# Optimization experiments

Hardware: AMD Instinct MI355X
Metric: run time of the kernel (lower is better)

## Reference

```python
import jax, jax.numpy as jnp
import numpy as np

B, N, V, D, C, H = 2, 4096, 4, 256, 3, 512


def setup_inputs() -> dict:
    key = jax.random.key(0)
    ks = jax.random.split(key, 8)
    desc = jax.random.normal(ks[0], (B, N, V, D), dtype=jnp.float32)
    sf = jax.random.normal(ks[1], (B, N, V, C), dtype=jnp.float32)
    T = jax.random.normal(ks[2], (V, 4, 4), dtype=jnp.float32)
    W1 = jax.random.normal(ks[3], (D, H), dtype=jnp.float32) * 0.05
    b1 = jnp.zeros((H,), dtype=jnp.float32)
    Wt = jax.random.normal(ks[4], (32, H), dtype=jnp.float32) * 0.05
    W2 = jax.random.normal(ks[5], (H, C), dtype=jnp.float32) * 0.05
    b2 = jnp.zeros((C,), dtype=jnp.float32)
    return {"desc": desc, "sf": sf, "T": T, "W1": W1, "b1": b1, "Wt": Wt, "W2": W2, "b2": b2}


def reference(desc, sf, T, W1, b1, Wt, W2, b2):
    # desc: [B,N,V,D], sf: [B,N,V,C], T: [V,4,4]
    Bn, Nn, Vn, Dn = desc.shape
    eps = 1e-12
    mutual = jnp.arange(Nn)[None, :]  # [1,N]

    def recon(d_i, Ti, Tj):
        # kpnet.reconstruction proxy: 2-layer MLP conditioned on flattened poses
        tcode = jnp.concatenate([Ti.ravel(), Tj.ravel()]) @ Wt  # [H]
        h = jax.nn.relu(d_i @ W1 + tcode + b1)                  # [B,N,H]
        return h @ W2 + b2                                      # [B,N,C]

    loss_total = jnp.float32(0.0)
    count = jnp.float32(0.0)
    for i in range(Vn):
        for j in range(Vn):
            if i == j:
                continue
            di = desc[:, :, i, :]  # [B,N,D]
            dj = desc[:, :, j, :]
            din = di / jnp.maximum(jnp.linalg.norm(di, axis=-1, keepdims=True), eps)
            djn = dj / jnp.maximum(jnp.linalg.norm(dj, axis=-1, keepdims=True), eps)
            sim_n = jnp.einsum('bnd,bmd->bnm', din, djn)  # [B,N,N]
            idx_ij = jnp.argmax(sim_n, axis=2)            # [B,N]
            idx_ji = jnp.argmax(sim_n, axis=1)            # [B,N]
            back = jnp.take_along_axis(idx_ji, idx_ij, axis=1)
            has_mutual = jnp.sum(back == mutual, axis=1) > 0  # [B]

            sf_recon = recon(di, T[i], T[j])              # [B,N,C]
            sim = jnp.einsum('bnd,bmd->bnm', di, dj)      # unnormalized, matches no_grad branch
            prob = jax.nn.softmax(sim, axis=2)
            sf_j_soft = jax.lax.stop_gradient(jnp.einsum('bnm,bmc->bnc', prob, sf[:, :, j, :]))
            loss_b = jnp.mean((sf_recon - sf_j_soft) ** 2, axis=(1, 2))  # [B]

            loss_total = loss_total + jnp.sum(jnp.where(has_mutual, loss_b, 0.0))
            count = count + jnp.sum(has_mutual.astype(jnp.float32))

    fallback = 0.0 * (W1.sum() + W2.sum() + Wt.sum() + b1.sum() + b2.sum())
    return jnp.where(count > 0, loss_total / jnp.maximum(count, 1.0), fallback)
```

## Files before the change

### kernel.cpp

```cpp
#include <hip/hip_runtime.h>
#include <cstdint>
#include <cstddef>

#define N_ 4096
#define B_ 2
#define V_ 4
#define D_ 256
#define C_ 3
#define H_ 512

#define PLANE 1048576
#define WPLANE 131072
#define NEG_INF (-__builtin_inff())
#define TSTRIDE 130

typedef __attribute__((ext_vector_type(8))) _Float16 f16x8;
typedef __attribute__((ext_vector_type(4))) float f32x4;

__device__ __forceinline__ void gload16(const void* g, void* l) {
    __builtin_amdgcn_global_load_lds(
        (const __attribute__((address_space(1))) void*)g,
        (__attribute__((address_space(3))) void*)l,
        16, 0, 0);
}

__device__ __forceinline__ void split2(float x, unsigned short& h, unsigned short& l) {
    _Float16 hh = (_Float16)x;
    float r = x - (float)hh;
    _Float16 ll = (_Float16)r;
    h = __builtin_bit_cast(unsigned short, hh);
    l = __builtin_bit_cast(unsigned short, ll);
}

__device__ __forceinline__ size_t sp_idx(int n, int d) {
    int R = n >> 4, rr = n & 15;
    int Kc = d >> 5, slot = (d >> 3) & 3, e = d & 7;
    return ((((size_t)R * 8 + Kc) * 4 + slot) * 16 + rr) * 8 + e;
}

__global__ __launch_bounds__(64) void zero_accum_kernel(float* loss_sum, int* hm) {
    int t = threadIdx.x;
    if (t < 24) loss_sum[t] = 0.0f;
    if (t < 12) hm[t] = 0;
}

__global__ __launch_bounds__(256) void split_kernel(const float* __restrict__ desc,
                                                    unsigned short* __restrict__ SP) {
    int t = blockIdx.x * 256 + threadIdx.x;
    int d4 = t & 63;
    int v  = (t >> 6) & 3;
    int n  = (t >> 8) & 4095;
    int b  = t >> 20;
    const float4 x = *(const float4*)(desc + (((size_t)(b * N_ + n) * V_ + v) << 8) + d4 * 4);
    ushort4 hv, lv;
    split2(x.x, hv.x, lv.x);
    split2(x.y, hv.y, lv.y);
    split2(x.z, hv.z, lv.z);
    split2(x.w, hv.w, lv.w);
    size_t base = (size_t)((b * V_ + v) * 2) * PLANE + sp_idx(n, d4 * 4);
    *(ushort4*)(SP + base)         = hv;
    *(ushort4*)(SP + base + PLANE) = lv;
}

__global__ __launch_bounds__(256) void w1split_kernel(const float* __restrict__ W1,
                                                      unsigned short* __restrict__ W1T) {
    int t = blockIdx.x * 256 + threadIdx.x;
    int h = t & 511;
    int k = t >> 9;
    float x = W1[(size_t)k * H_ + h];
    unsigned short hv, lv;
    split2(x, hv, lv);
    size_t o = sp_idx(h, k);
    W1T[o] = hv; W1T[o + WPLANE] = lv;
}

__global__ __launch_bounds__(256) void norms_kernel(const float* __restrict__ desc,
                                                    float* __restrict__ invn) {
    int gw   = (blockIdx.x * 256 + threadIdx.x) >> 6;
    int lane = threadIdx.x & 63;
    int bv = gw >> 12;
    int n  = gw & (N_ - 1);
    int b  = bv >> 2, v = bv & 3;
    const float* p = desc + ((size_t)(b * N_ + n) * V_ + v) * D_;
    float4 x = *(const float4*)(p + lane * 4);
    float s = x.x * x.x + x.y * x.y + x.z * x.z + x.w * x.w;
    #pragma unroll
    for (int off = 32; off >= 1; off >>= 1) s += __shfl_xor(s, off, 64);
    if (lane == 0) invn[gw] = 1.0f / fmaxf(sqrtf(s), 1e-12f);
}

__global__ __launch_bounds__(256) void fgram_kernel(
    const unsigned short* __restrict__ SP,
    const float* __restrict__ sf,
    const float* __restrict__ invn,
    float* __restrict__ PT) {
    __shared__ __align__(16) unsigned char smraw[49152];
    __shared__ float wmax[4];
    unsigned short* stage = (unsigned short*)smraw;
    float* tile  = (float*)smraw;
    float* CSb   = (float*)(smraw + 33280);
    float4* sfj4 = (float4*)(smraw + 37888);
    float4* sfi4 = (float4*)(smraw + 41984);

    const int tid = threadIdx.x;
    const int wid = tid >> 6, lane = tid & 63;
    const int wr = wid >> 1, wc = wid & 1;
    const int g = lane >> 4, ccol = lane & 15;

    const int pi[6] = {0, 0, 0, 1, 1, 2}, pj[6] = {1, 2, 3, 2, 3, 3};
    const int u = blockIdx.y, b = u & 1;
    const int i = pi[u >> 1], j = pj[u >> 1];
    float* RP = PT + (size_t)u * 64 * N_ * 8;
    float* CP = RP + (size_t)32 * N_ * 8;

    const int bid = blockIdx.x;
    const int swz = (bid & 7) * 64 + (bid >> 3);
    const int strip = swz >> 4, chunk = swz & 15;
    const int n0 = strip * 128, m0 = chunk * 256;

    const unsigned short* Ahi = SP + (size_t)((b * V_ + i) * 2 + 0) * PLANE;
    const unsigned short* Alo = Ahi + PLANE;
    const unsigned short* Bhi = SP + (size_t)((b * V_ + j) * 2 + 0) * PLANE;
    const unsigned short* Blo = Bhi + PLANE;
    const int gA = b * V_ + i, gB = b * V_ + j;

    const int q = wid * 2;

    for (int t = 0; t < 2; ++t) {
        const int brow0 = m0 + t * 128;
        const int RA0 = n0 >> 4, RB0 = brow0 >> 4;

        f32x4 acc[4][4];
        #pragma unroll
        for (int m = 0; m < 4; ++m)
            #pragma unroll
            for (int n = 0; n < 4; ++n) acc[m][n] = (f32x4){0.f, 0.f, 0.f, 0.f};

        for (int k0 = 0; k0 < D_; k0 += 32) {
            const int Kc = k0 >> 5;
            __syncthreads();
            const unsigned short* planes[4] = {Ahi, Alo, Bhi, Blo};
            #pragma unroll
            for (int pl = 0; pl < 4; ++pl) {
                const int R0 = (pl < 2) ? RA0 : RB0;
                #pragma unroll
                for (int c = 0; c < 2; ++c) {
                    const unsigned short* gp =
                        planes[pl] + (((size_t)(R0 + q + c) * 8 + Kc) * 512) + lane * 8;
                    gload16(gp, stage + pl * 4096 + (q + c) * 512);
                }
            }
            __syncthreads();

            const int funit = (g * 16 + ccol) * 8;
            f16x8 ah[4], al4[4], bh[4];
            #pragma unroll
            for (int m = 0; m < 4; ++m) {
                ah[m]  = *(const f16x8*)(stage + 0 * 4096 + (wr * 4 + m) * 512 + funit);
                al4[m] = *(const f16x8*)(stage + 1 * 4096 + (wr * 4 + m) * 512 + funit);
                bh[m]  = *(const f16x8*)(stage + 2 * 4096 + (wc * 4 + m) * 512 + funit);
            }
            #pragma unroll
            for (int m = 0; m < 4; ++m)
                #pragma unroll
                for (int n = 0; n < 4; ++n)
                    acc[m][n] = __builtin_amdgcn_mfma_f32_16x16x32_f16(
                        ah[m], bh[n], acc[m][n], 0, 0, 0);
            #pragma unroll
            for (int m = 0; m < 4; ++m)
                #pragma unroll
                for (int n = 0; n < 4; ++n)
                    acc[m][n] = __builtin_amdgcn_mfma_f32_16x16x32_f16(
                        al4[m], bh[n], acc[m][n], 0, 0, 0);
            f16x8 bl4[4];
            #pragma unroll
            for (int n = 0; n < 4; ++n)
                bl4[n] = *(const f16x8*)(stage + 3 * 4096 + (wc * 4 + n) * 512 + funit);
            #pragma unroll
            for (int m = 0; m < 4; ++m)
                #pragma unroll
                for (int n = 0; n < 4; ++n)
                    acc[m][n] = __builtin_amdgcn_mfma_f32_16x16x32_f16(
                        ah[m], bl4[n], acc[m][n], 0, 0, 0);
        }

        float tmax = NEG_INF;
        #pragma unroll
        for (int m = 0; m < 4; ++m)
            #pragma unroll
            for (int n = 0; n < 4; ++n)
                #pragma unroll
                for (int r = 0; r < 4; ++r)
                    tmax = fmaxf(tmax, acc[m][n][r]);
        #pragma unroll
        for (int off = 1; off <= 32; off <<= 1)
            tmax = fmaxf(tmax, __shfl_xor(tmax, off, 64));
        if (lane == 0) wmax[wid] = tmax;
        __syncthreads();
        const float mxt = fmaxf(fmaxf(wmax[0], wmax[1]), fmaxf(wmax[2], wmax[3]));

        {
            if (tid < 128) {
                int m = m0 + t * 128 + tid;
                const float* p = sf + (((size_t)(b * N_ + m)) * V_ + j) * C_;
                sfj4[tid] = make_float4(p[0], p[1], p[2], invn[(size_t)gB * N_ + m]);
            } else {
                int n = n0 + (tid & 127);
                const float* p = sf + (((size_t)(b * N_ + n)) * V_ + i) * C_;
                sfi4[tid & 127] = make_float4(p[0], p[1], p[2], invn[(size_t)gA * N_ + n]);
            }
        }

        for (int half = 0; half < 2; ++half) {
            if (wr == half) {
                #pragma unroll
                for (int m = 0; m < 4; ++m)
                    #pragma unroll
                    for (int nf = 0; nf < 4; ++nf) {
                        int c = wc * 64 + nf * 16 + ccol;
                        int rb = m * 16 + g * 4;
                        #pragma unroll
                        for (int r = 0; r < 4; ++r)
                            tile[(rb + r) * TSTRIDE + c] = acc[m][nf][r];
                    }
            }
            __syncthreads();

            {
                const int row = tid >> 2, qq = tid & 3;
                const float* rp = tile + row * TSTRIDE;
                float sum = 0.f, w0 = 0.f, w1 = 0.f, w2 = 0.f;
                float bv = NEG_INF, bif = (float)N_;
                for (int ii = 0; ii < 32; ++ii) {
                    int c = (ii << 2) + qq;
                    float s = rp[c];
                    float4 sp = sfj4[c];
                    float e = __expf(s - mxt);
                    sum += e;
                    w0 = fmaf(e, sp.x, w0); w1 = fmaf(e, sp.y, w1); w2 = fmaf(e, sp.z, w2);
                    float vv = s * sp.w;
                    float gi = (float)(m0 + t * 128 + c);
                    if (vv > bv || (vv == bv && gi < bif)) { bv = vv; bif = gi; }
                }
                #pragma unroll
                for (int off = 1; off <= 2; off <<= 1) {
                    sum += __shfl_xor(sum, off, 64);
                    w0  += __shfl_xor(w0, off, 64);
                    w1  += __shfl_xor(w1, off, 64);
                    w2  += __shfl_xor(w2, off, 64);
                    float ob = __shfl_xor(bv, off, 64);
                    float oi = __shfl_xor(bif, off, 64);
                    if (ob > bv || (ob == bv && oi < bif)) { bv = ob; bif = oi; }
                }
                if (qq == 0) {
                    float* o = RP + ((size_t)(chunk * 2 + t) * N_ + n0 + half * 64 + row) * 8;
                    *(float4*)o       = make_float4(mxt, sum, w0, w1);
                    *(float4*)(o + 4) = make_float4(w2, bv, bif, 0.f);
                }
            }

            {
                const int c = tid >> 1, h = tid & 1;
                const float* cp = tile + (h * 32) * TSTRIDE + c;
                const int rb0 = half * 64 + h * 32;
                float sum = 0.f, w0 = 0.f, w1 = 0.f, w2 = 0.f;
                float bv = NEG_INF, bif = (float)N_;
                for (int ii = 0; ii < 32; ++ii) {
                    float s = cp[ii * TSTRIDE];
                    float4 sp = sfi4[rb0 + ii];
                    float e = __expf(s - mxt);
                    sum += e;
                    w0 = fmaf(e, sp.x, w0); w1 = fmaf(e, sp.y, w1); w2 = fmaf(e, sp.z, w2);
                    float vv = s * sp.w;
                    float gi = (float)(n0 + rb0 + ii);
                    if (vv > bv || (vv == bv && gi < bif)) { bv = vv; bif = gi; }
                }
                {
                    sum += __shfl_xor(sum, 1, 64);
                    w0  += __shfl_xor(w0, 1, 64);
                    w1  += __shfl_xor(w1, 1, 64);
                    w2  += __shfl_xor(w2, 1, 64);
                    float ob = __shfl_xor(bv, 1, 64);
                    float oi = __shfl_xor(bif, 1, 64);
                    if (ob > bv || (ob == bv && oi < bif)) { bv = ob; bif = oi; }
                }
                if (h == 0) {
                    float* cs = CSb + c * 9;
                    if (half == 0) {
                        cs[0] = sum; cs[1] = w0; cs[2] = w1; cs[3] = w2;
                        cs[4] = bv;  cs[5] = bif;
                    } else {
                        cs[0] += sum; cs[1] += w0; cs[2] += w1; cs[3] += w2;
                        if (bv > cs[4] || (bv == cs[4] && bif < cs[5])) { cs[4] = bv; cs[5] = bif; }
                    }
                }
            }
            __syncthreads();
        }

        if (tid < 128) {
            const float* cs = CSb + tid * 9;
            float* o = CP + ((size_t)strip * N_ + m0 + t * 128 + tid) * 8;
            *(float4*)o       = make_float4(mxt, cs[0], cs[1], cs[2]);
            *(float4*)(o + 4) = make_float4(cs[3], cs[4], cs[5], 0.f);
        }
    }
}

__global__ __launch_bounds__(256) void comb_kernel(const float* __restrict__ PT,
                                                   float* __restrict__ soft,
                                                   int* __restrict__ idxbuf) {
    const int pi[6] = {0, 0, 0, 1, 1, 2}, pj[6] = {1, 2, 3, 2, 3, 3};
    int u = blockIdx.y, p = u >> 1, b = u & 1;
    int i = pi[p], j = pj[p];
    int x = blockIdx.x;
    int idx = (x & 15) * 256 + threadIdx.x;
    const size_t unit = (size_t)u * 64 * N_ * 8;
    const float* base;
    int dd, which;
    if (x < 16) { base = PT + unit + (size_t)idx * 8;                       dd = (i * 3 + (j - 1)) * 2 + b; which = 0; }
    else        { base = PT + unit + (size_t)32 * N_ * 8 + (size_t)idx * 8; dd = (j * 3 + i) * 2 + b;       which = 1; }

    float4 a = *(const float4*)base;
    float4 b4 = *(const float4*)(base + 4);
    float M = a.x, S = a.y, w0 = a.z, w1 = a.w, w2 = b4.x, av = b4.y, ai = b4.z;
    for (int k = 1; k < 32; ++k) {
        const float* qp = base + (size_t)k * N_ * 8;
        float4 c = *(const float4*)qp;
        float4 d = *(const float4*)(qp + 4);
        if (c.x > M) {
            float e = __expf(M - c.x);
            M = c.x;
            S  = fmaf(S,  e, c.y);
            w0 = fmaf(w0, e, c.z);
            w1 = fmaf(w1, e, c.w);
            w2 = fmaf(w2, e, d.x);
        } else {
            float e = __expf(c.x - M);
            S  = fmaf(c.y, e, S);
            w0 = fmaf(c.z, e, w0);
            w1 = fmaf(c.w, e, w1);
            w2 = fmaf(d.x, e, w2);
        }
        if (d.y > av || (d.y == av && d.z < ai)) { av = d.y; ai = d.z; }
    }
    float inv = 1.0f / S;
    float* so = soft + ((size_t)dd * N_ + idx) * 3;
    so[0] = w0 * inv; so[1] = w1 * inv; so[2] = w2 * inv;
    idxbuf[((size_t)u * 2 + which) * N_ + idx] = (int)ai;
}

__global__ __launch_bounds__(256) void mutualB_kernel(const int* __restrict__ idxbuf,
                                                      int* __restrict__ hm) {
    int u = blockIdx.y;
    int n = blockIdx.x * 256 + threadIdx.x;
    int a = idxbuf[((size_t)u * 2 + 0) * N_ + n];
    int ok = (idxbuf[((size_t)u * 2 + 1) * N_ + a] == n) ? 1 : 0;
    unsigned long long m = __ballot(ok);
    if ((threadIdx.x & 63) == 0 && m != 0ull) atomicOr(&hm[u], 1);
}

__global__ __launch_bounds__(256) void zmm3_kernel(const unsigned short* __restrict__ SP,
                                                   const unsigned short* __restrict__ W1T,
                                                   const float* __restrict__ b1,
                                                   float* __restrict__ Z) {
    __shared__ __align__(16) unsigned short stage[4 * 4096];
    const int tid = threadIdx.x;
    const int wid = tid >> 6, lane = tid & 63;
    const int wr = wid >> 1, wc = wid & 1;
    const int g = lane >> 4, ccol = lane & 15;
    const int bv = blockIdx.z;
    const int arow0 = blockIdx.x * 128, bcol0 = blockIdx.y * 128;
    const int RA0 = arow0 >> 4, RB0 = bcol0 >> 4;

    const unsigned short* Ahi = SP + (size_t)(bv * 2) * PLANE;
    const unsigned short* Alo = Ahi + PLANE;
    const unsigned short* Bhi = W1T;
    const unsigned short* Blo = W1T + WPLANE;
    float* Cout = Z + (size_t)bv * N_ * H_;

    f32x4 acc[4][4];
    #pragma unroll
    for (int m = 0; m < 4; ++m)
        #pragma unroll
        for (int n = 0; n < 4; ++n) acc[m][n] = (f32x4){0.f, 0.f, 0.f, 0.f};

    const int q = wid * 2;

    for (int k0 = 0; k0 < D_; k0 += 32) {
        const int Kc = k0 >> 5;
        __syncthreads();
        const unsigned short* planes[4] = {Ahi, Alo, Bhi, Blo};
        #pragma unroll
        for (int pl = 0; pl < 4; ++pl) {
            const int R0 = (pl < 2) ? RA0 : RB0;
            #pragma unroll
            for (int c = 0; c < 2; ++c) {
                const unsigned short* gp =
                    planes[pl] + (((size_t)(R0 + q + c) * 8 + Kc) * 512) + lane * 8;
                gload16(gp, stage + pl * 4096 + (q + c) * 512);
            }
        }
        __syncthreads();

        const int funit = (g * 16 + ccol) * 8;
        f16x8 ah[4], al4[4], bh[4];
        #pragma unroll
        for (int m = 0; m < 4; ++m) {
            ah[m]  = *(const f16x8*)(stage + 0 * 4096 + (wr * 4 + m) * 512 + funit);
            al4[m] = *(const f16x8*)(stage + 1 * 4096 + (wr * 4 + m) * 512 + funit);
            bh[m]  = *(const f16x8*)(stage + 2 * 4096 + (wc * 4 + m) * 512 + funit);
        }
        #pragma unroll
        for (int m = 0; m < 4; ++m)
            #pragma unroll
            for (int n = 0; n < 4; ++n)
                acc[m][n] = __builtin_amdgcn_mfma_f32_16x16x32_f16(ah[m], bh[n], acc[m][n], 0, 0, 0);
        #pragma unroll
        for (int m = 0; m < 4; ++m)
            #pragma unroll
            for (int n = 0; n < 4; ++n)
                acc[m][n] = __builtin_amdgcn_mfma_f32_16x16x32_f16(al4[m], bh[n], acc[m][n], 0, 0, 0);
        f16x8 bl4[4];
        #pragma unroll
        for (int n = 0; n < 4; ++n)
            bl4[n] = *(const f16x8*)(stage + 3 * 4096 + (wc * 4 + n) * 512 + funit);
        #pragma unroll
        for (int m = 0; m < 4; ++m)
            #pragma unroll
            for (int n = 0; n < 4; ++n)
                acc[m][n] = __builtin_amdgcn_mfma_f32_16x16x32_f16(ah[m], bl4[n], acc[m][n], 0, 0, 0);
    }

    const int crow = (lane >> 4) * 4;
    #pragma unroll
    for (int m = 0; m < 4; ++m) {
        const int gr = arow0 + wr * 64 + m * 16 + crow;
        #pragma unroll
        for (int n = 0; n < 4; ++n) {
            const int gc = bcol0 + wc * 64 + n * 16 + ccol;
            f32x4 v = acc[m][n];
            float bvx = b1[gc];
            #pragma unroll
            for (int r = 0; r < 4; ++r)
                Cout[(size_t)(gr + r) * H_ + gc] = v[r] + bvx;
        }
    }
}

__global__ __launch_bounds__(512) void tcode_kernel(const float* __restrict__ T,
                                                    const float* __restrict__ Wt,
                                                    float* __restrict__ tcode) {
    int dp = blockIdx.x;
    int i = dp / 3, rem = dp % 3;
    int j = rem + (rem >= i ? 1 : 0);
    int h = threadIdx.x;
    float acc = 0.0f;
    #pragma unroll
    for (int k = 0; k < 16; k++) acc = fmaf(T[i * 16 + k], Wt[k * H_ + h], acc);
    #pragma unroll
    for (int k = 0; k < 16; k++) acc = fmaf(T[j * 16 + k], Wt[(16 + k) * H_ + h], acc);
    tcode[dp * H_ + h] = acc;
}

__global__ __launch_bounds__(256) void loss_kernel(const float* __restrict__ Z,
                                                   const float* __restrict__ tcode,
                                                   const float* __restrict__ soft,
                                                   const float* __restrict__ W2,
                                                   const float* __restrict__ b2,
                                                   float* __restrict__ loss_sum) {
    int dd = blockIdx.y;
    int dp = dd >> 1, b = dd & 1;
    int i = dp / 3;
    const float* tc = tcode + (size_t)dp * H_;
    const float* zbase = Z + (size_t)((b * V_ + i) * N_) * H_;
    const float* softb = soft + (size_t)dd * N_ * C_;
    int tid = threadIdx.x;
    int wid = tid >> 6, lane = tid & 63;
    __shared__ float wsum[4];
    float sse_acc = 0.0f;
    float4 t1 = *(const float4*)(tc + lane * 4);
    float4 t2 = *(const float4*)(tc + 256 + lane * 4);
    for (int rr = wid; rr < 64; rr += 4) {
        int n = blockIdx.x * 64 + rr;
        const float* zp = zbase + (size_t)n * H_;
        float4 z1 = *(const float4*)(zp + lane * 4);
        float4 z2 = *(const float4*)(zp + 256 + lane * 4);
        float pre[8] = {z1.x + t1.x, z1.y + t1.y, z1.z + t1.z, z1.w + t1.w,
                        z2.x + t2.x, z2.y + t2.y, z2.z + t2.z, z2.w + t2.w};
        float c0 = 0.f, c1 = 0.f, c2 = 0.f;
        int h1 = lane * 4, h2 = 256 + lane * 4;
        #pragma unroll
        for (int q = 0; q < 8; q++) {
            float rv = fmaxf(pre[q], 0.0f);
            int h = (q < 4) ? (h1 + q) : (h2 + q - 4);
            c0 = fmaf(rv, W2[h * 3 + 0], c0);
            c1 = fmaf(rv, W2[h * 3 + 1], c1);
            c2 = fmaf(rv, W2[h * 3 + 2], c2);
        }
        #pragma unroll
        for (int off = 32; off >= 1; off >>= 1) {
            c0 += __shfl_xor(c0, off, 64);
            c1 += __shfl_xor(c1, off, 64);
            c2 += __shfl_xor(c2, off, 64);
        }
        if (lane == 0) {
            float e0 = c0 + b2[0] - softb[(size_t)n * C_ + 0];
            float e1 = c1 + b2[1] - softb[(size_t)n * C_ + 1];
            float e2 = c2 + b2[2] - softb[(size_t)n * C_ + 2];
            sse_acc += e0 * e0 + e1 * e1 + e2 * e2;
        }
    }
    if (lane == 0) wsum[wid] = sse_acc;
    __syncthreads();
    if (tid == 0) {
        atomicAdd(&loss_sum[dd], wsum[0] + wsum[1] + wsum[2] + wsum[3]);
    }
}

__global__ __launch_bounds__(64) void final_kernel(const float* __restrict__ loss_sum,
                                                   const int* __restrict__ hm,
                                                   float* __restrict__ out) {
    if (threadIdx.x != 0 || blockIdx.x != 0) return;
    float lt = 0.0f, cnt = 0.0f;
    for (int dp = 0; dp < 12; dp++) {
        int i = dp / 3, rem = dp % 3;
        int j = rem + (rem >= i ? 1 : 0);
        int a = i < j ? i : j, c = i < j ? j : i;
        int p = a * 3 - (a * (a - 1)) / 2 + (c - a - 1);
        for (int b = 0; b < 2; b++) {
            if (hm[p * 2 + b]) {
                lt += loss_sum[dp * 2 + b] * (1.0f / ((float)N_ * (float)C_));
                cnt += 1.0f;
            }
        }
    }
    out[0] = (cnt > 0.0f) ? (lt / cnt) : 0.0f;
}

extern "C" void kernel_launch(void* const* d_in, const int* in_sizes, int n_in,
                              void* d_out, int out_size, void* d_ws, size_t ws_size,
                              hipStream_t stream) {
    const float* desc = (const float*)d_in[0];
    const float* sf   = (const float*)d_in[1];
    const float* T    = (const float*)d_in[2];
    const float* W1   = (const float*)d_in[3];
    const float* b1   = (const float*)d_in[4];
    const float* Wt   = (const float*)d_in[5];
    const float* W2   = (const float*)d_in[6];
    const float* b2   = (const float*)d_in[7];
    float* out = (float*)d_out;

    const size_t NM = (size_t)N_ * N_;
    unsigned short* SP  = (unsigned short*)d_ws;
    unsigned short* W1T = SP + (size_t)16 * PLANE;
    float* w     = (float*)(W1T + (size_t)2 * WPLANE);
    float* Z     = w;
    float* PT    = w + NM;
    float* invn  = PT + (size_t)12 * 64 * N_ * 8;
    float* tcode = invn + (size_t)B_ * V_ * N_;
    float* soft  = tcode + 12 * H_;
    int*   idxbuf = (int*)(soft + (size_t)12 * B_ * N_ * C_);
    float* loss_sum = (float*)(idxbuf + (size_t)12 * 2 * N_);
    int*   hm    = (int*)(loss_sum + 24);

    zero_accum_kernel<<<1, 64, 0, stream>>>(loss_sum, hm);
    split_kernel<<<8192, 256, 0, stream>>>(desc, SP);
    w1split_kernel<<<512, 256, 0, stream>>>(W1, W1T);
    norms_kernel<<<(B_ * V_ * N_) / 4, 256, 0, stream>>>(desc, invn);
    tcode_kernel<<<12, 512, 0, stream>>>(T, Wt, tcode);

    fgram_kernel<<<dim3(512, 12), 256, 0, stream>>>(SP, sf, invn, PT);

    zmm3_kernel<<<dim3(32, 4, 8), 256, 0, stream>>>(SP, W1T, b1, Z);
    comb_kernel<<<dim3(32, 12), 256, 0, stream>>>(PT, soft, idxbuf);
    mutualB_kernel<<<dim3(16, 12), 256, 0, stream>>>(idxbuf, hm);
    loss_kernel<<<dim3(64, 24), 256, 0, stream>>>(Z, tcode, soft, W2, b2, loss_sum);
    final_kernel<<<1, 64, 0, stream>>>(loss_sum, hm, out);
}
```

Before: 1.172 ms.

## Double K-step staging in fgram and reuse exponentials for column softmax

Widens the K chunk staged per sync from 32 to 64, halving the number of barrier-separated load/compute rounds. Shared memory grows to about 64KB of dynamic LDS, which may reduce occupancy. The row pass now writes exp values back into the tile so the column pass reuses them instead of recomputing expf. The column argmax is computed from the register accumulators with warp shuffles instead of from the shared tile, at the cost of an extra barrier.

```diff
diff --git a/kernel.cpp b/kernel.cpp
--- a/kernel.cpp
+++ b/kernel.cpp
@@ -94,13 +94,13 @@
     const float* __restrict__ sf,
     const float* __restrict__ invn,
     float* __restrict__ PT) {
-    __shared__ __align__(16) unsigned char smraw[49152];
-    __shared__ float wmax[4];
+    extern __shared__ __align__(16) unsigned char smraw[];
     unsigned short* stage = (unsigned short*)smraw;
     float* tile  = (float*)smraw;
     float* CSb   = (float*)(smraw + 33280);
     float4* sfj4 = (float4*)(smraw + 37888);
     float4* sfi4 = (float4*)(smraw + 41984);
+    float* wmax  = (float*)(smraw + 65536);
 
     const int tid = threadIdx.x;
     const int wid = tid >> 6, lane = tid & 63;
@@ -136,52 +136,57 @@
             #pragma unroll
             for (int n = 0; n < 4; ++n) acc[m][n] = (f32x4){0.f, 0.f, 0.f, 0.f};
 
-        for (int k0 = 0; k0 < D_; k0 += 32) {
-            const int Kc = k0 >> 5;
+        for (int k0 = 0; k0 < D_; k0 += 64) {
+            const int Kc0 = k0 >> 5;
             __syncthreads();
             const unsigned short* planes[4] = {Ahi, Alo, Bhi, Blo};
             #pragma unroll
             for (int pl = 0; pl < 4; ++pl) {
                 const int R0 = (pl < 2) ? RA0 : RB0;
                 #pragma unroll
-                for (int c = 0; c < 2; ++c) {
+                for (int c = 0; c < 4; ++c) {
+                    const int rowg = q + (c >> 1);
+                    const int kc = c & 1;
                     const unsigned short* gp =
-                        planes[pl] + (((size_t)(R0 + q + c) * 8 + Kc) * 512) + lane * 8;
-                    gload16(gp, stage + pl * 4096 + (q + c) * 512);
+                        planes[pl] + (((size_t)(R0 + rowg) * 8 + Kc0 + kc) * 512) + lane * 8;
+                    gload16(gp, stage + pl * 8192 + (rowg * 2 + kc) * 512);
                 }
             }
             __syncthreads();
 
             const int funit = (g * 16 + ccol) * 8;
-            f16x8 ah[4], al4[4], bh[4];
-            #pragma unroll
-            for (int m = 0; m < 4; ++m) {
-                ah[m]  = *(const f16x8*)(stage + 0 * 4096 + (wr * 4 + m) * 512 + funit);
-                al4[m] = *(const f16x8*)(stage + 1 * 4096 + (wr * 4 + m) * 512 + funit);
-                bh[m]  = *(const f16x8*)(stage + 2 * 4096 + (wc * 4 + m) * 512 + funit);
-            }
-            #pragma unroll
-            for (int m = 0; m < 4; ++m)
+            #pragma unroll
+            for (int kk2 = 0; kk2 < 2; ++kk2) {
+                f16x8 ah[4], al4[4], bh4[4];
+                #pragma unroll
+                for (int m = 0; m < 4; ++m) {
+                    ah[m]  = *(const f16x8*)(stage + 0 * 8192 + ((wr * 4 + m) * 2 + kk2) * 512 + funit);
+                    al4[m] = *(const f16x8*)(stage + 1 * 8192 + ((wr * 4 + m) * 2 + kk2) * 512 + funit);
+                    bh4[m] = *(const f16x8*)(stage + 2 * 8192 + ((wc * 4 + m) * 2 + kk2) * 512 + funit);
+                }
+                #pragma unroll
+                for (int m = 0; m < 4; ++m)
+                    #pragma unroll
+                    for (int n = 0; n < 4; ++n)
+                        acc[m][n] = __builtin_amdgcn_mfma_f32_16x16x32_f16(
+                            ah[m], bh4[n], acc[m][n], 0, 0, 0);
+                #pragma unroll
+                for (int m = 0; m < 4; ++m)
+                    #pragma unroll
+                    for (int n = 0; n < 4; ++n)
+                        acc[m][n] = __builtin_amdgcn_mfma_f32_16x16x32_f16(
+                            al4[m], bh4[n], acc[m][n], 0, 0, 0);
+                f16x8 bl4[4];
                 #pragma unroll
                 for (int n = 0; n < 4; ++n)
-                    acc[m][n] = __builtin_amdgcn_mfma_f32_16x16x32_f16(
-                        ah[m], bh[n], acc[m][n], 0, 0, 0);
-            #pragma unroll
-            for (int m = 0; m < 4; ++m)
-                #pragma unroll
-                for (int n = 0; n < 4; ++n)
-                    acc[m][n] = __builtin_amdgcn_mfma_f32_16x16x32_f16(
-                        al4[m], bh[n], acc[m][n], 0, 0, 0);
-            f16x8 bl4[4];
-            #pragma unroll
-            for (int n = 0; n < 4; ++n)
-                bl4[n] = *(const f16x8*)(stage + 3 * 4096 + (wc * 4 + n) * 512 + funit);
-            #pragma unroll
-            for (int m = 0; m < 4; ++m)
-                #pragma unroll
-                for (int n = 0; n < 4; ++n)
-                    acc[m][n] = __builtin_amdgcn_mfma_f32_16x16x32_f16(
-                        ah[m], bl4[n], acc[m][n], 0, 0, 0);
+                    bl4[n] = *(const f16x8*)(stage + 3 * 8192 + ((wc * 4 + n) * 2 + kk2) * 512 + funit);
+                #pragma unroll
+                for (int m = 0; m < 4; ++m)
+                    #pragma unroll
+                    for (int n = 0; n < 4; ++n)
+                        acc[m][n] = __builtin_amdgcn_mfma_f32_16x16x32_f16(
+                            ah[m], bl4[n], acc[m][n], 0, 0, 0);
+            }
         }
 
         float tmax = NEG_INF;
@@ -228,7 +233,7 @@
 
             {
                 const int row = tid >> 2, qq = tid & 3;
-                const float* rp = tile + row * TSTRIDE;
+                float* rp = tile + row * TSTRIDE;
                 float sum = 0.f, w0 = 0.f, w1 = 0.f, w2 = 0.f;
                 float bv = NEG_INF, bif = (float)N_;
                 for (int ii = 0; ii < 32; ++ii) {
@@ -241,6 +246,7 @@
                     float vv = s * sp.w;
                     float gi = (float)(m0 + t * 128 + c);
                     if (vv > bv || (vv == bv && gi < bif)) { bv = vv; bif = gi; }
+                    rp[c] = e;
                 }
                 #pragma unroll
                 for (int off = 1; off <= 2; off <<= 1) {
@@ -258,40 +264,73 @@
                     *(float4*)(o + 4) = make_float4(w2, bv, bif, 0.f);
                 }
             }
+            __syncthreads();
 
             {
                 const int c = tid >> 1, h = tid & 1;
                 const float* cp = tile + (h * 32) * TSTRIDE + c;
                 const int rb0 = half * 64 + h * 32;
                 float sum = 0.f, w0 = 0.f, w1 = 0.f, w2 = 0.f;
-                float bv = NEG_INF, bif = (float)N_;
                 for (int ii = 0; ii < 32; ++ii) {
-                    float s = cp[ii * TSTRIDE];
+                    float e = cp[ii * TSTRIDE];
                     float4 sp = sfi4[rb0 + ii];
-                    float e = __expf(s - mxt);
                     sum += e;
                     w0 = fmaf(e, sp.x, w0); w1 = fmaf(e, sp.y, w1); w2 = fmaf(e, sp.z, w2);
-                    float vv = s * sp.w;
-                    float gi = (float)(n0 + rb0 + ii);
-                    if (vv > bv || (vv == bv && gi < bif)) { bv = vv; bif = gi; }
-                }
-                {
-                    sum += __shfl_xor(sum, 1, 64);
-                    w0  += __shfl_xor(w0, 1, 64);
-                    w1  += __shfl_xor(w1, 1, 64);
-                    w2  += __shfl_xor(w2, 1, 64);
-                    float ob = __shfl_xor(bv, 1, 64);
-                    float oi = __shfl_xor(bif, 1, 64);
-                    if (ob > bv || (ob == bv && oi < bif)) { bv = ob; bif = oi; }
-                }
+                }
+                sum += __shfl_xor(sum, 1, 64);
+                w0  += __shfl_xor(w0, 1, 64);
+                w1  += __shfl_xor(w1, 1, 64);
+                w2  += __shfl_xor(w2, 1, 64);
                 if (h == 0) {
                     float* cs = CSb + c * 9;
                     if (half == 0) {
                         cs[0] = sum; cs[1] = w0; cs[2] = w1; cs[3] = w2;
-                        cs[4] = bv;  cs[5] = bif;
                     } else {
                         cs[0] += sum; cs[1] += w0; cs[2] += w1; cs[3] += w2;
-                        if (bv > cs[4] || (bv == cs[4] && bif < cs[5])) { cs[4] = bv; cs[5] = bif; }
+                    }
+                }
+            }
+
+            if (wr == half) {
+                float bv4[4] = {NEG_INF, NEG_INF, NEG_INF, NEG_INF};
+                float bi4[4] = {(float)N_, (float)N_, (float)N_, (float)N_};
+                #pragma unroll
+                for (int m = 0; m < 4; ++m)
+                    #pragma unroll
+                    for (int r = 0; r < 4; ++r) {
+                        int row = half * 64 + m * 16 + g * 4 + r;
+                        float iv = sfi4[row].w;
+                        float gn = (float)(n0 + row);
+                        #pragma unroll
+                        for (int nf = 0; nf < 4; ++nf) {
+                            float vv = acc[m][nf][r] * iv;
+                            if (vv > bv4[nf] || (vv == bv4[nf] && gn < bi4[nf])) {
+                                bv4[nf] = vv; bi4[nf] = gn;
+                            }
+                        }
+                    }
+                #pragma unroll
+                for (int nf = 0; nf < 4; ++nf) {
+                    #pragma unroll
+                    for (int off = 16; off <= 32; off <<= 1) {
+                        float ob = __shfl_xor(bv4[nf], off, 64);
+                        float oi = __shfl_xor(bi4[nf], off, 64);
+                        if (ob > bv4[nf] || (ob == bv4[nf] && oi < bi4[nf])) {
+                            bv4[nf] = ob; bi4[nf] = oi;
+                        }
+                    }
+                }
+                if (g == 0) {
+                    #pragma unroll
+                    for (int nf = 0; nf < 4; ++nf) {
+                        float* cs = CSb + (wc * 64 + nf * 16 + ccol) * 9;
+                        if (half == 0) {
+                            cs[4] = bv4[nf]; cs[5] = bi4[nf];
+                        } else {
+                            if (bv4[nf] > cs[4] || (bv4[nf] == cs[4] && bi4[nf] < cs[5])) {
+                                cs[4] = bv4[nf]; cs[5] = bi4[nf];
+                            }
+                        }
                     }
                 }
             }
@@ -570,7 +609,7 @@
     norms_kernel<<<(B_ * V_ * N_) / 4, 256, 0, stream>>>(desc, invn);
     tcode_kernel<<<12, 512, 0, stream>>>(T, Wt, tcode);
 
-    fgram_kernel<<<dim3(512, 12), 256, 0, stream>>>(SP, sf, invn, PT);
+    fgram_kernel<<<dim3(512, 12), 256, 65552, stream>>>(SP, sf, invn, PT);
 
     zmm3_kernel<<<dim3(32, 4, 8), 256, 0, stream>>>(SP, W1T, b1, Z);
     comb_kernel<<<dim3(32, 12), 256, 0, stream>>>(PT, soft, idxbuf);
```

Result: slower. 1.323 ms (+12.9%).
